# Performance work log

Measured on AMD Instinct MI355X. Metric: run time of the kernel, lower is better.

## Reference

```python
import jax, jax.numpy as jnp
import numpy as np

N_NODES = 100000
N_EDGES = 1600000
D_IN = 128
D_HID = 128
D_OUT = 64


def setup_inputs() -> dict:
    key = jax.random.key(0)
    ks = jax.random.split(key, 8)
    x = jax.random.normal(ks[0], (N_NODES, D_IN), dtype=jnp.float32)
    edge_index = jax.random.randint(ks[1], (2, N_EDGES), 0, N_NODES, dtype=jnp.int64)
    s1 = 1.0 / np.sqrt(D_IN)
    s2 = 1.0 / np.sqrt(D_HID)
    W1 = jax.random.uniform(ks[2], (D_IN, D_HID), jnp.float32, -s1, s1)
    b1 = jnp.zeros((D_HID,), jnp.float32)
    W2 = jax.random.uniform(ks[3], (D_HID, D_HID), jnp.float32, -s2, s2)
    b2 = jnp.zeros((D_HID,), jnp.float32)
    fc_W = jax.random.uniform(ks[4], (D_HID, D_OUT), jnp.float32, -s2, s2)
    fc_b = jax.random.uniform(ks[5], (D_OUT,), jnp.float32, -s2, s2)
    return {"x": x, "edge_index": edge_index, "W1": W1, "b1": b1,
            "W2": W2, "b2": b2, "fc_W": fc_W, "fc_b": fc_b}


def _gcn_norm(edge_index, n_nodes):
    # add self-loops, compute symmetric normalization D^{-1/2} A D^{-1/2}
    loops = jnp.arange(n_nodes, dtype=edge_index.dtype)
    src = jnp.concatenate([edge_index[0], loops])  # [E+N]
    dst = jnp.concatenate([edge_index[1], loops])
    ones = jnp.ones(src.shape[0], jnp.float32)
    deg = jax.ops.segment_sum(ones, dst, num_segments=n_nodes)  # [N]
    dinv = 1.0 / jnp.sqrt(deg)  # deg >= 1 thanks to self-loops
    norm = dinv[src] * dinv[dst]  # [E+N]
    return src, dst, norm


def _gcn_conv(x, W, b, src, dst, norm, n_nodes):
    h = x @ W                                  # [N, d]
    msg = h[src] * norm[:, None]               # gather + scale, [E+N, d]
    out = jax.ops.segment_sum(msg, dst, num_segments=n_nodes)  # scatter-add
    return out + b


def reference(x, edge_index, W1, b1, W2, b2, fc_W, fc_b):
    n = x.shape[0]
    src, dst, norm = _gcn_norm(edge_index, n)
    h = jax.nn.relu(_gcn_conv(x, W1, b1, src, dst, norm, n))
    # dropout is identity in inference mode
    h = jax.nn.relu(_gcn_conv(h, W2, b2, src, dst, norm, n))
    return h @ fc_W + fc_b
```

## Files before the change

### kernel.cpp

```cpp
#include <hip/hip_runtime.h>

typedef __attribute__((ext_vector_type(8))) short bf16x8;
typedef __attribute__((ext_vector_type(4))) float f32x4;
typedef __attribute__((ext_vector_type(2))) float f32x2;

__device__ __forceinline__ unsigned short f2bf(float x) {
  union { float f; unsigned u; } v; v.f = x;
  return (unsigned short)((v.u + 0x7fffu + ((v.u >> 16) & 1u)) >> 16);
}


__global__ __launch_bounds__(256) void bhist_k(const int* __restrict__ dst,
                                               int* __restrict__ bcnt, int E, int B) {
  __shared__ int h[512];
  for (int i = threadIdx.x; i < B; i += 256) h[i] = 0;
  __syncthreads();
  for (int e = blockIdx.x * 256 + threadIdx.x; e < E; e += gridDim.x * 256)
    atomicAdd(&h[dst[e] >> 8], 1);
  __syncthreads();
  for (int i = threadIdx.x; i < B; i += 256)
    if (h[i]) atomicAdd(&bcnt[i * 16], h[i]);
}

__global__ __launch_bounds__(256) void bin_k(const int* __restrict__ src,
                                             const int* __restrict__ dst,
                                             const int* __restrict__ bcnt,
                                             int* __restrict__ bfill,
                                             unsigned* __restrict__ ebuf, int E, int B) {
  __shared__ int hist[512];
  __shared__ int base[512];
  __shared__ int sd[256];
  int t = threadIdx.x;
  int i0 = 2 * t, i1 = 2 * t + 1;
  int v0 = (i0 < B) ? bcnt[i0 * 16] : 0;
  int v1 = (i1 < B) ? bcnt[i1 * 16] : 0;
  int ts = v0 + v1;
  sd[t] = ts; __syncthreads();
  for (int off = 1; off < 256; off <<= 1) {
    int x = (t >= off) ? sd[t - off] : 0;
    __syncthreads();
    sd[t] += x;
    __syncthreads();
  }
  int excl = sd[t] - ts;
  base[i0] = excl;
  base[i1] = excl + v0;
  __syncthreads();

  int chunk = (E + gridDim.x - 1) / gridDim.x;
  int e0 = blockIdx.x * chunk;
  int e1 = e0 + chunk; if (e1 > E) e1 = E;
  for (int i = t; i < B; i += 256) hist[i] = 0;
  __syncthreads();
  for (int e = e0 + t; e < e1; e += 256) atomicAdd(&hist[dst[e] >> 8], 1);
  __syncthreads();
  for (int i = t; i < B; i += 256) {
    int c = hist[i];
    hist[i] = base[i] + (c ? atomicAdd(&bfill[i * 16], c) : 0);
  }
  __syncthreads();
  for (int e = e0 + t; e < e1; e += 256) {
    int d = dst[e];
    int b = d >> 8;
    int pos = atomicAdd(&hist[b], 1);
    ebuf[pos] = ((unsigned)(d & 255) << 17) | (unsigned)src[e];
  }
}

__global__ __launch_bounds__(256) void bsort_k(const unsigned* __restrict__ ebuf,
                                               const int* __restrict__ bcnt,
                                               int* __restrict__ csr,
                                               int* __restrict__ row_start,
                                               float* __restrict__ dinv, int N, int B, int E) {
  __shared__ int cnt[256];
  __shared__ int sd[256];
  __shared__ int ofs[256];
  __shared__ int sorted[8192];
  __shared__ int s_bs, s_m;
  int b = blockIdx.x, t = threadIdx.x;
  int i0 = 2 * t, i1 = 2 * t + 1;
  int v0 = (i0 < B) ? bcnt[i0 * 16] : 0;
  int v1 = (i1 < B) ? bcnt[i1 * 16] : 0;
  int ts = v0 + v1;
  sd[t] = ts; __syncthreads();
  for (int off = 1; off < 256; off <<= 1) {
    int x = (t >= off) ? sd[t - off] : 0;
    __syncthreads();
    sd[t] += x;
    __syncthreads();
  }
  int excl = sd[t] - ts;
  if (i0 == b) { s_bs = excl; s_m = v0; }
  if (i1 == b) { s_bs = excl + v0; s_m = v1; }
  if (b == 0 && t == 0) row_start[N] = E;
  __syncthreads();
  int bs = s_bs, m = s_m;
  if (m > 8192) m = 8192;

  cnt[t] = 0;
  __syncthreads();
  for (int i = t; i < m; i += 256) atomicAdd(&cnt[ebuf[bs + i] >> 17], 1);
  __syncthreads();
  int deg = cnt[t];
  sd[t] = deg; __syncthreads();
  for (int off = 1; off < 256; off <<= 1) {
    int x = (t >= off) ? sd[t - off] : 0;
    __syncthreads();
    sd[t] += x;
    __syncthreads();
  }
  int nexcl = sd[t] - deg;
  ofs[t] = nexcl;
  int node = (b << 8) + t;
  if (node < N) {
    row_start[node] = bs + nexcl;
    dinv[node] = rsqrtf((float)(deg + 1));
  }
  __syncthreads();
  for (int i = t; i < m; i += 256) {
    unsigned r = ebuf[bs + i];
    int d = r >> 17;
    int p = atomicAdd(&ofs[d], 1);
    if (p < 8192) sorted[p] = (int)(r & 0x1FFFFu);
  }
  __syncthreads();
  for (int i = t; i < m; i += 256) csr[bs + i] = sorted[i];
}

template <int NCOL, bool INF32, bool OUTF32, bool SCALE>
__global__ __launch_bounds__(256) void gemm_k(const void* __restrict__ Ap,
                                              const float* __restrict__ W,
                                              const float* __restrict__ bias,
                                              const float* __restrict__ rowscale,
                                              void* __restrict__ Cp, int M) {
  __shared__ __align__(16) unsigned short Ws[NCOL * 136];
  int tid = threadIdx.x;
  for (int e = tid; e < 128 * NCOL; e += 256) {
    int k = e / NCOL, n = e % NCOL;
    Ws[n * 136 + k] = f2bf(W[e]);
  }
  __syncthreads();

  int wave = tid >> 6, lane = tid & 63;
  int q = lane >> 4, r = lane & 15;
  const int NT = NCOL / 16;
  int ntile = M >> 4;
  for (int tile = blockIdx.x * 4 + wave; tile < ntile; tile += gridDim.x * 4) {
    int row = tile * 16 + r;
    bf16x8 a[4];
    if (INF32) {
      const float* A = (const float*)Ap + (size_t)row * 128 + q * 8;
#pragma unroll
      for (int kk = 0; kk < 4; kk++) {
        const float4* p = (const float4*)(A + kk * 32);
        float4 f0 = p[0], f1 = p[1];
        bf16x8 tt;
        tt[0] = (short)f2bf(f0.x); tt[1] = (short)f2bf(f0.y);
        tt[2] = (short)f2bf(f0.z); tt[3] = (short)f2bf(f0.w);
        tt[4] = (short)f2bf(f1.x); tt[5] = (short)f2bf(f1.y);
        tt[6] = (short)f2bf(f1.z); tt[7] = (short)f2bf(f1.w);
        a[kk] = tt;
      }
    } else {
      const unsigned short* A = (const unsigned short*)Ap + (size_t)row * 128 + q * 8;
#pragma unroll
      for (int kk = 0; kk < 4; kk++) a[kk] = *(const bf16x8*)(A + kk * 32);
    }
    f32x4 acc[NT];
#pragma unroll
    for (int nt = 0; nt < NT; nt++) { acc[nt][0] = 0.f; acc[nt][1] = 0.f; acc[nt][2] = 0.f; acc[nt][3] = 0.f; }
#pragma unroll
    for (int kk = 0; kk < 4; kk++) {
#pragma unroll
      for (int nt = 0; nt < NT; nt++) {
        bf16x8 bfr = *(const bf16x8*)&Ws[(nt * 16 + r) * 136 + kk * 32 + q * 8];
        acc[nt] = __builtin_amdgcn_mfma_f32_16x16x32_bf16(a[kk], bfr, acc[nt], 0, 0, 0);
      }
    }
#pragma unroll
    for (int rr = 0; rr < 4; rr++) {
      int orow = tile * 16 + q * 4 + rr;
      float rs = SCALE ? rowscale[orow] : 1.f;
#pragma unroll
      for (int nt = 0; nt < NT; nt++) {
        int ocol = nt * 16 + r;
        if (OUTF32)
          ((float*)Cp)[(size_t)orow * NCOL + ocol] = acc[nt][rr] + bias[ocol];
        else
          ((unsigned short*)Cp)[(size_t)orow * NCOL + ocol] = f2bf(acc[nt][rr] * rs);
      }
    }
  }
}

__global__ __launch_bounds__(256) void agg_k(const unsigned short* __restrict__ hs,
                                             const float* __restrict__ dinv,
                                             const int* __restrict__ row_start,
                                             const int* __restrict__ csr,
                                             const float* __restrict__ bias,
                                             unsigned short* __restrict__ out, int N) {
  int lane = threadIdx.x & 63;
  int node = (blockIdx.x * 256 + threadIdx.x) >> 6;
  if (node >= N) return;
  float di = dinv[node];
  int beg = row_start[node];
  int deg = row_start[node + 1] - beg;

  const unsigned short* colp = hs + lane * 2;

  f32x2 acc; acc[0] = 0.f; acc[1] = 0.f;

  for (int base = -1; base < deg; base += 64) {
    int idx = base + lane;
    int s = node;
    if (idx >= 0 && idx < deg) s = csr[beg + idx];
    int cntv = deg - base; if (cntv > 64) cntv = 64;
    int j = 0;
    for (; j + 16 <= cntv; j += 16) {
      unsigned u[16];
#pragma unroll
      for (int k = 0; k < 16; k++) {
        int sj = __builtin_amdgcn_readlane(s, j + k);
        u[k] = *(const unsigned*)(colp + (size_t)sj * 128);
      }
#pragma unroll
      for (int k = 0; k < 16; k++) {
        f32x2 p;
        p[0] = __uint_as_float(u[k] << 16);
        p[1] = __uint_as_float(u[k] & 0xffff0000u);
        acc += p;
      }
    }
    if (j < cntv) {
      unsigned u[16];
      float w[16];
#pragma unroll
      for (int k = 0; k < 16; k++) {
        int sj = __builtin_amdgcn_readlane(s, (j + k) & 63);
        u[k] = *(const unsigned*)(colp + (size_t)sj * 128);
        w[k] = (j + k < cntv) ? 1.f : 0.f;
      }
#pragma unroll
      for (int k = 0; k < 16; k++) {
        f32x2 p;
        p[0] = __uint_as_float(u[k] << 16);
        p[1] = __uint_as_float(u[k] & 0xffff0000u);
        f32x2 wv; wv[0] = w[k]; wv[1] = w[k];
        acc += p * wv;
      }
    }
  }

  f32x2 bv = *(const f32x2*)(bias + lane * 2);
  float v0 = acc[0] * di + bv[0];
  float v1 = acc[1] * di + bv[1];
  if (v0 < 0.f) v0 = 0.f;
  if (v1 < 0.f) v1 = 0.f;
  unsigned pk = ((unsigned)f2bf(v1) << 16) | (unsigned)f2bf(v0);
  *(unsigned*)(out + (size_t)node * 128 + lane * 2) = pk;
}

extern "C" void kernel_launch(void* const* d_in, const int* in_sizes, int n_in,
                              void* d_out, int out_size, void* d_ws, size_t ws_size,
                              hipStream_t stream) {
  const float* x  = (const float*)d_in[0];
  const int* ei   = (const int*)d_in[1];
  const float* W1 = (const float*)d_in[2];
  const float* b1 = (const float*)d_in[3];
  const float* W2 = (const float*)d_in[4];
  const float* b2 = (const float*)d_in[5];
  const float* fcW = (const float*)d_in[6];
  const float* fcb = (const float*)d_in[7];
  float* out = (float*)d_out;

  int N = in_sizes[0] / 128;
  int E = in_sizes[1] / 2;
  int B = (N + 255) >> 8;
  const int* src = ei;
  const int* dst = ei + E;

  char* w = (char*)d_ws;
  auto alloc = [&](size_t b) { char* p = w; w += (b + 255) & ~(size_t)255; return p; };
  float* dinv      = (float*)alloc((size_t)N * 4);
  int*   row_start = (int*)alloc((size_t)(N + 1) * 4);
  int*   batom     = (int*)alloc((size_t)(B + 1) * 128);
  int*   bcnt      = batom;
  int*   bfill     = batom + (size_t)(B + 1) * 16;
  unsigned* ebuf   = (unsigned*)alloc((size_t)E * 4);
  int*   csr       = (int*)alloc((size_t)E * 4);
  unsigned short* bufA = (unsigned short*)alloc((size_t)N * 128 * 2);
  unsigned short* bufB = (unsigned short*)alloc((size_t)N * 128 * 2);

  hipMemsetAsync(batom, 0, (size_t)(B + 1) * 128, stream);

  bhist_k<<<256, 256, 0, stream>>>(dst, bcnt, E, B);
  bin_k<<<256, 256, 0, stream>>>(src, dst, bcnt, bfill, ebuf, E, B);
  bsort_k<<<B, 256, 0, stream>>>(ebuf, bcnt, csr, row_start, dinv, N, B, E);

  gemm_k<128, true, false, true><<<782, 256, 0, stream>>>((const void*)x, W1, nullptr, dinv,
                                                          (void*)bufA, N);
  agg_k<<<(N + 3) / 4, 256, 0, stream>>>(bufA, dinv, row_start, csr, b1, bufB, N);
  gemm_k<128, false, false, true><<<782, 256, 0, stream>>>((const void*)bufB, W2, nullptr, dinv,
                                                           (void*)bufA, N);
  agg_k<<<(N + 3) / 4, 256, 0, stream>>>(bufA, dinv, row_start, csr, b2, bufB, N);
  gemm_k<64, false, true, false><<<782, 256, 0, stream>>>((const void*)bufB, fcW, fcb, nullptr,
                                                          (void*)out, N);
}
```

Measured before the change: 333.9 us.

## Fuse first GEMM with edge histogram and replace atomics with per-block partial histograms

New measurement: 349.3 us. 4.6% more time.

```diff
diff --git a/kernel.cpp b/kernel.cpp
--- a/kernel.cpp
+++ b/kernel.cpp
@@ -9,56 +9,124 @@
   return (unsigned short)((v.u + 0x7fffu + ((v.u >> 16) & 1u)) >> 16);
 }
 
-
-__global__ __launch_bounds__(256) void bhist_k(const int* __restrict__ dst,
-                                               int* __restrict__ bcnt, int E, int B) {
-  __shared__ int h[512];
-  for (int i = threadIdx.x; i < B; i += 256) h[i] = 0;
-  __syncthreads();
-  for (int e = blockIdx.x * 256 + threadIdx.x; e < E; e += gridDim.x * 256)
-    atomicAdd(&h[dst[e] >> 8], 1);
-  __syncthreads();
-  for (int i = threadIdx.x; i < B; i += 256)
-    if (h[i]) atomicAdd(&bcnt[i * 16], h[i]);
+__global__ __launch_bounds__(256) void g1hist_k(const float* __restrict__ x,
+                                                const float* __restrict__ W,
+                                                unsigned short* __restrict__ C, int M,
+                                                const int* __restrict__ dst,
+                                                int* __restrict__ phist, int E, int B,
+                                                int G1) {
+  __shared__ __align__(16) unsigned short Ws[128 * 136];
+  int tid = threadIdx.x;
+
+  if ((int)blockIdx.x < 256) {
+    int i = blockIdx.x;
+    int* h = (int*)Ws;
+    for (int b = tid; b < B; b += 256) h[b] = 0;
+    __syncthreads();
+    int chunk = (E + 255) / 256;
+    int e0 = i * chunk;
+    int e1 = e0 + chunk; if (e1 > E) e1 = E;
+    for (int e = e0 + tid; e < e1; e += 256) atomicAdd(&h[dst[e] >> 8], 1);
+    __syncthreads();
+    for (int b = tid; b < B; b += 256) phist[i * B + b] = h[b];
+    return;
+  }
+
+  for (int e = tid; e < 128 * 128; e += 256) {
+    int k = e / 128, n = e % 128;
+    Ws[n * 136 + k] = f2bf(W[e]);
+  }
+  __syncthreads();
+
+  int wave = tid >> 6, lane = tid & 63;
+  int q = lane >> 4, r = lane & 15;
+  int ntile = M >> 4;
+  int bid = blockIdx.x - 256;
+  for (int tile = bid * 4 + wave; tile < ntile; tile += G1 * 4) {
+    int row = tile * 16 + r;
+    bf16x8 a[4];
+    const float* A = x + (size_t)row * 128 + q * 8;
+#pragma unroll
+    for (int kk = 0; kk < 4; kk++) {
+      const float4* p = (const float4*)(A + kk * 32);
+      float4 f0 = p[0], f1 = p[1];
+      bf16x8 tt;
+      tt[0] = (short)f2bf(f0.x); tt[1] = (short)f2bf(f0.y);
+      tt[2] = (short)f2bf(f0.z); tt[3] = (short)f2bf(f0.w);
+      tt[4] = (short)f2bf(f1.x); tt[5] = (short)f2bf(f1.y);
+      tt[6] = (short)f2bf(f1.z); tt[7] = (short)f2bf(f1.w);
+      a[kk] = tt;
+    }
+    f32x4 acc[8];
+#pragma unroll
+    for (int nt = 0; nt < 8; nt++) { acc[nt][0] = 0.f; acc[nt][1] = 0.f; acc[nt][2] = 0.f; acc[nt][3] = 0.f; }
+#pragma unroll
+    for (int kk = 0; kk < 4; kk++) {
+#pragma unroll
+      for (int nt = 0; nt < 8; nt++) {
+        bf16x8 bfr = *(const bf16x8*)&Ws[(nt * 16 + r) * 136 + kk * 32 + q * 8];
+        acc[nt] = __builtin_amdgcn_mfma_f32_16x16x32_bf16(a[kk], bfr, acc[nt], 0, 0, 0);
+      }
+    }
+#pragma unroll
+    for (int rr = 0; rr < 4; rr++) {
+      int orow = tile * 16 + q * 4 + rr;
+#pragma unroll
+      for (int nt = 0; nt < 8; nt++) {
+        int ocol = nt * 16 + r;
+        C[(size_t)orow * 128 + ocol] = f2bf(acc[nt][rr]);
+      }
+    }
+  }
 }
 
 __global__ __launch_bounds__(256) void bin_k(const int* __restrict__ src,
                                              const int* __restrict__ dst,
-                                             const int* __restrict__ bcnt,
-                                             int* __restrict__ bfill,
+                                             const int* __restrict__ phist,
+                                             int* __restrict__ gbase,
+                                             int* __restrict__ btot,
                                              unsigned* __restrict__ ebuf, int E, int B) {
   __shared__ int hist[512];
-  __shared__ int base[512];
+  __shared__ int pre[512];
+  __shared__ int tot[512];
   __shared__ int sd[256];
   int t = threadIdx.x;
+  int j = blockIdx.x;
+
+  for (int b = t; b < 512; b += 256) { pre[b] = 0; tot[b] = 0; }
+  __syncthreads();
+  for (int b = t; b < B; b += 256) {
+    int s = 0, p = 0;
+    for (int i = 0; i < 256; i++) {
+      if (i == j) p = s;
+      s += phist[i * B + b];
+    }
+    pre[b] = p;
+    tot[b] = s;
+  }
+  __syncthreads();
   int i0 = 2 * t, i1 = 2 * t + 1;
-  int v0 = (i0 < B) ? bcnt[i0 * 16] : 0;
-  int v1 = (i1 < B) ? bcnt[i1 * 16] : 0;
+  int v0 = tot[i0], v1 = tot[i1];
   int ts = v0 + v1;
   sd[t] = ts; __syncthreads();
   for (int off = 1; off < 256; off <<= 1) {
-    int x = (t >= off) ? sd[t - off] : 0;
-    __syncthreads();
-    sd[t] += x;
+    int xx = (t >= off) ? sd[t - off] : 0;
+    __syncthreads();
+    sd[t] += xx;
     __syncthreads();
   }
   int excl = sd[t] - ts;
-  base[i0] = excl;
-  base[i1] = excl + v0;
-  __syncthreads();
-
-  int chunk = (E + gridDim.x - 1) / gridDim.x;
-  int e0 = blockIdx.x * chunk;
+  hist[i0] = excl + pre[i0];
+  hist[i1] = excl + v0 + pre[i1];
+  if (j == 0) {
+    if (i0 < B) { gbase[i0] = excl;      btot[i0] = v0; }
+    if (i1 < B) { gbase[i1] = excl + v0; btot[i1] = v1; }
+  }
+  __syncthreads();
+
+  int chunk = (E + 255) / 256;
+  int e0 = j * chunk;
   int e1 = e0 + chunk; if (e1 > E) e1 = E;
-  for (int i = t; i < B; i += 256) hist[i] = 0;
-  __syncthreads();
-  for (int e = e0 + t; e < e1; e += 256) atomicAdd(&hist[dst[e] >> 8], 1);
-  __syncthreads();
-  for (int i = t; i < B; i += 256) {
-    int c = hist[i];
-    hist[i] = base[i] + (c ? atomicAdd(&bfill[i * 16], c) : 0);
-  }
-  __syncthreads();
   for (int e = e0 + t; e < e1; e += 256) {
     int d = dst[e];
     int b = d >> 8;
@@ -68,7 +136,8 @@
 }
 
 __global__ __launch_bounds__(256) void bsort_k(const unsigned* __restrict__ ebuf,
-                                               const int* __restrict__ bcnt,
+                                               const int* __restrict__ gbase,
+                                               const int* __restrict__ btot,
                                                int* __restrict__ csr,
                                                int* __restrict__ row_start,
                                                float* __restrict__ dinv, int N, int B, int E) {
@@ -76,25 +145,10 @@
   __shared__ int sd[256];
   __shared__ int ofs[256];
   __shared__ int sorted[8192];
-  __shared__ int s_bs, s_m;
   int b = blockIdx.x, t = threadIdx.x;
-  int i0 = 2 * t, i1 = 2 * t + 1;
-  int v0 = (i0 < B) ? bcnt[i0 * 16] : 0;
-  int v1 = (i1 < B) ? bcnt[i1 * 16] : 0;
-  int ts = v0 + v1;
-  sd[t] = ts; __syncthreads();
-  for (int off = 1; off < 256; off <<= 1) {
-    int x = (t >= off) ? sd[t - off] : 0;
-    __syncthreads();
-    sd[t] += x;
-    __syncthreads();
-  }
-  int excl = sd[t] - ts;
-  if (i0 == b) { s_bs = excl; s_m = v0; }
-  if (i1 == b) { s_bs = excl + v0; s_m = v1; }
+  int bs = gbase[b];
+  int m = btot[b];
   if (b == 0 && t == 0) row_start[N] = E;
-  __syncthreads();
-  int bs = s_bs, m = s_m;
   if (m > 8192) m = 8192;
 
   cnt[t] = 0;
@@ -127,7 +181,7 @@
   for (int i = t; i < m; i += 256) csr[bs + i] = sorted[i];
 }
 
-template <int NCOL, bool INF32, bool OUTF32, bool SCALE>
+template <int NCOL, bool OUTF32, bool SCALE>
 __global__ __launch_bounds__(256) void gemm_k(const void* __restrict__ Ap,
                                               const float* __restrict__ W,
                                               const float* __restrict__ bias,
@@ -148,24 +202,9 @@
   for (int tile = blockIdx.x * 4 + wave; tile < ntile; tile += gridDim.x * 4) {
     int row = tile * 16 + r;
     bf16x8 a[4];
-    if (INF32) {
-      const float* A = (const float*)Ap + (size_t)row * 128 + q * 8;
-#pragma unroll
-      for (int kk = 0; kk < 4; kk++) {
-        const float4* p = (const float4*)(A + kk * 32);
-        float4 f0 = p[0], f1 = p[1];
-        bf16x8 tt;
-        tt[0] = (short)f2bf(f0.x); tt[1] = (short)f2bf(f0.y);
-        tt[2] = (short)f2bf(f0.z); tt[3] = (short)f2bf(f0.w);
-        tt[4] = (short)f2bf(f1.x); tt[5] = (short)f2bf(f1.y);
-        tt[6] = (short)f2bf(f1.z); tt[7] = (short)f2bf(f1.w);
-        a[kk] = tt;
-      }
-    } else {
-      const unsigned short* A = (const unsigned short*)Ap + (size_t)row * 128 + q * 8;
-#pragma unroll
-      for (int kk = 0; kk < 4; kk++) a[kk] = *(const bf16x8*)(A + kk * 32);
-    }
+    const unsigned short* A = (const unsigned short*)Ap + (size_t)row * 128 + q * 8;
+#pragma unroll
+    for (int kk = 0; kk < 4; kk++) a[kk] = *(const bf16x8*)(A + kk * 32);
     f32x4 acc[NT];
 #pragma unroll
     for (int nt = 0; nt < NT; nt++) { acc[nt][0] = 0.f; acc[nt][1] = 0.f; acc[nt][2] = 0.f; acc[nt][3] = 0.f; }
@@ -193,6 +232,7 @@
   }
 }
 
+template <bool ESCALE>
 __global__ __launch_bounds__(256) void agg_k(const unsigned short* __restrict__ hs,
                                              const float* __restrict__ dinv,
                                              const int* __restrict__ row_start,
@@ -218,17 +258,20 @@
     int j = 0;
     for (; j + 16 <= cntv; j += 16) {
       unsigned u[16];
+      float dv[16];
 #pragma unroll
       for (int k = 0; k < 16; k++) {
         int sj = __builtin_amdgcn_readlane(s, j + k);
         u[k] = *(const unsigned*)(colp + (size_t)sj * 128);
+        if (ESCALE) dv[k] = dinv[sj];
       }
 #pragma unroll
       for (int k = 0; k < 16; k++) {
         f32x2 p;
         p[0] = __uint_as_float(u[k] << 16);
         p[1] = __uint_as_float(u[k] & 0xffff0000u);
-        acc += p;
+        if (ESCALE) { acc[0] += p[0] * dv[k]; acc[1] += p[1] * dv[k]; }
+        else        { acc += p; }
       }
     }
     if (j < cntv) {
@@ -239,14 +282,15 @@
         int sj = __builtin_amdgcn_readlane(s, (j + k) & 63);
         u[k] = *(const unsigned*)(colp + (size_t)sj * 128);
         w[k] = (j + k < cntv) ? 1.f : 0.f;
+        if (ESCALE) w[k] *= dinv[sj];
       }
 #pragma unroll
       for (int k = 0; k < 16; k++) {
         f32x2 p;
         p[0] = __uint_as_float(u[k] << 16);
         p[1] = __uint_as_float(u[k] & 0xffff0000u);
-        f32x2 wv; wv[0] = w[k]; wv[1] = w[k];
-        acc += p * wv;
+        acc[0] += p[0] * w[k];
+        acc[1] += p[1] * w[k];
       }
     }
   }
@@ -283,26 +327,23 @@
   auto alloc = [&](size_t b) { char* p = w; w += (b + 255) & ~(size_t)255; return p; };
   float* dinv      = (float*)alloc((size_t)N * 4);
   int*   row_start = (int*)alloc((size_t)(N + 1) * 4);
-  int*   batom     = (int*)alloc((size_t)(B + 1) * 128);
-  int*   bcnt      = batom;
-  int*   bfill     = batom + (size_t)(B + 1) * 16;
+  int*   phist     = (int*)alloc((size_t)256 * B * 4);
+  int*   gbase     = (int*)alloc((size_t)B * 4);
+  int*   btot      = (int*)alloc((size_t)B * 4);
   unsigned* ebuf   = (unsigned*)alloc((size_t)E * 4);
   int*   csr       = (int*)alloc((size_t)E * 4);
   unsigned short* bufA = (unsigned short*)alloc((size_t)N * 128 * 2);
   unsigned short* bufB = (unsigned short*)alloc((size_t)N * 128 * 2);
 
-  hipMemsetAsync(batom, 0, (size_t)(B + 1) * 128, stream);
-
-  bhist_k<<<256, 256, 0, stream>>>(dst, bcnt, E, B);
-  bin_k<<<256, 256, 0, stream>>>(src, dst, bcnt, bfill, ebuf, E, B);
-  bsort_k<<<B, 256, 0, stream>>>(ebuf, bcnt, csr, row_start, dinv, N, B, E);
-
-  gemm_k<128, true, false, true><<<782, 256, 0, stream>>>((const void*)x, W1, nullptr, dinv,
-                                                          (void*)bufA, N);
-  agg_k<<<(N + 3) / 4, 256, 0, stream>>>(bufA, dinv, row_start, csr, b1, bufB, N);
-  gemm_k<128, false, false, true><<<782, 256, 0, stream>>>((const void*)bufB, W2, nullptr, dinv,
-                                                           (void*)bufA, N);
-  agg_k<<<(N + 3) / 4, 256, 0, stream>>>(bufA, dinv, row_start, csr, b2, bufB, N);
-  gemm_k<64, false, true, false><<<782, 256, 0, stream>>>((const void*)bufB, fcW, fcb, nullptr,
-                                                          (void*)out, N);
-}
+  const int G1 = 782;
+
+  g1hist_k<<<256 + G1, 256, 0, stream>>>(x, W1, bufA, N, dst, phist, E, B, G1);
+  bin_k<<<256, 256, 0, stream>>>(src, dst, phist, gbase, btot, ebuf, E, B);
+  bsort_k<<<B, 256, 0, stream>>>(ebuf, gbase, btot, csr, row_start, dinv, N, B, E);
+  agg_k<true><<<(N + 3) / 4, 256, 0, stream>>>(bufA, dinv, row_start, csr, b1, bufB, N);
+  gemm_k<128, false, true><<<782, 256, 0, stream>>>((const void*)bufB, W2, nullptr, dinv,
+                                                    (void*)bufA, N);
+  agg_k<false><<<(N + 3) / 4, 256, 0, stream>>>(bufA, dinv, row_start, csr, b2, bufB, N);
+  gemm_k<64, true, false><<<782, 256, 0, stream>>>((const void*)bufB, fcW, fcb, nullptr,
+                                                   (void*)out, N);
+}
```
